# Optimization experiments

Hardware: AMD Instinct MI355X
Metric: run time of the kernel (lower is better)

Reference implementation:

```python
import jax, jax.numpy as jnp
import numpy as np


def _glorot(key, shape):
    fan_in, fan_out = shape[0], shape[1]
    lim = float(np.sqrt(6.0 / (fan_in + fan_out)))
    return jax.random.uniform(key, shape, jnp.float32, -lim, lim)


def setup_inputs() -> dict:
    key = jax.random.key(0)
    ks = jax.random.split(key, 17)
    B, P, F = 32, 9045, 750  # batch, pairs-per-subject, feature dim
    x = jax.random.normal(ks[0], (B, P, F), jnp.float32)
    # SimilarityMeasureNetwork: 750 -> 32 -> 16 -> 8 -> 1
    sw1 = _glorot(ks[1], (750, 32)); sb1 = jnp.zeros((32,), jnp.float32)
    sw2 = _glorot(ks[2], (32, 16));  sb2 = jnp.zeros((16,), jnp.float32)
    sw3 = _glorot(ks[3], (16, 8));   sb3 = jnp.zeros((8,), jnp.float32)
    sw4 = _glorot(ks[4], (8, 1));    sb4 = jnp.zeros((1,), jnp.float32)
    # ClassificationNet: 9045 -> 1024 -> 256 -> 64 -> 3
    cw1 = _glorot(ks[5], (9045, 1024)); cb1 = jnp.zeros((1024,), jnp.float32)
    cw2 = _glorot(ks[6], (1024, 256));  cb2 = jnp.zeros((256,), jnp.float32)
    cw3 = _glorot(ks[7], (256, 64));    cb3 = jnp.zeros((64,), jnp.float32)
    cw4 = _glorot(ks[8], (64, 3));      cb4 = jnp.zeros((3,), jnp.float32)
    return dict(x=x, sw1=sw1, sb1=sb1, sw2=sw2, sb2=sb2, sw3=sw3, sb3=sb3,
                sw4=sw4, sb4=sb4, cw1=cw1, cb1=cb1, cw2=cw2, cb2=cb2,
                cw3=cw3, cb3=cb3, cw4=cw4, cb4=cb4)


def reference(x, sw1, sb1, sw2, sb2, sw3, sb3, sw4, sb4,
              cw1, cb1, cw2, cb2, cw3, cb3, cw4, cb4):
    # Similarity MLP, batched over all (subject, pair) rows at once.
    # Dropout layers are identity at inference.
    h = jax.nn.relu(jnp.einsum('bpf,fk->bpk', x, sw1) + sb1)   # [B,P,32]
    h = jax.nn.relu(h @ sw2 + sb2)                              # [B,P,16]
    h = jax.nn.relu(h @ sw3 + sb3)                              # [B,P,8]
    sim = jnp.tanh(h @ sw4 + sb4)[..., 0]                        # [B,P]
    # Classification MLP on the per-subject similarity vector.
    c = jax.nn.relu(sim @ cw1 + cb1)                             # [B,1024]
    c = jax.nn.relu(c @ cw2 + cb2)                               # [B,256]
    c = jax.nn.relu(c @ cw3 + cb3)                               # [B,64]
    logits = c @ cw4 + cb4                                       # [B,3]
    return jax.nn.log_softmax(logits, axis=1)
```

## Files before the change

kernel.cpp:

```cpp
#include <hip/hip_runtime.h>
#include <stdint.h>
#include <stddef.h>

#define BB 32
#define PP 9045
#define FF 750
#define MM (BB*PP)
#define NT16 (MM/16)

typedef float  f32x4  __attribute__((ext_vector_type(4)));
typedef short  s16x8  __attribute__((ext_vector_type(8)));
typedef unsigned int u32x4v __attribute__((ext_vector_type(4)));

__device__ __forceinline__ unsigned rne_bf16(float f){
    unsigned u = __builtin_bit_cast(unsigned, f);
    return (u + 0x7fffu + ((u >> 16) & 1u)) >> 16;
}
__device__ __forceinline__ unsigned pack2(float lo, float hi){
    return rne_bf16(lo) | (rne_bf16(hi) << 16);
}
__device__ __forceinline__ float tanh_fast(float v){
    return 1.f - 2.f / (1.f + __expf(2.f * v));
}

__global__ void k_w1f(const float* __restrict__ sw1, u32x4v* __restrict__ w1f){
    int t = blockIdx.x * blockDim.x + threadIdx.x;
    if (t >= 24*2*64) return;
    int lane = t & 63, nt = (t >> 6) & 1, s = t >> 7;
    int col = nt*16 + (lane & 15);
    int kb  = s*32 + ((lane >> 4) << 3);
    float v[8];
    #pragma unroll
    for (int e = 0; e < 8; ++e){ int k = kb + e; v[e] = (k < FF) ? sw1[k*32 + col] : 0.f; }
    u32x4v o;
    o.x = pack2(v[0],v[1]); o.y = pack2(v[2],v[3]);
    o.z = pack2(v[4],v[5]); o.w = pack2(v[6],v[7]);
    w1f[t] = o;
}

__global__ __launch_bounds__(256) void k_sim(
    const float* __restrict__ x, const u32x4v* __restrict__ w1f,
    const float* __restrict__ sb1,
    const float* __restrict__ sw2, const float* __restrict__ sb2,
    const float* __restrict__ sw3, const float* __restrict__ sb3,
    const float* __restrict__ sw4, const float* __restrict__ sb4,
    float* __restrict__ simT)
{
    __shared__ __align__(16) unsigned short h1buf[4][16*40];
    __shared__ __align__(16) unsigned short h2buf[4][16*40];
    const int wid  = threadIdx.x >> 6;
    const int lane = threadIdx.x & 63;
    for (int i = lane; i < 16*40; i += 64) h2buf[wid][i] = 0;
    const int tile = blockIdx.x*4 + wid;
    if (tile >= NT16) return;
    const int g = lane >> 4;
    const int c = lane & 15;
    const int r0 = tile << 4;
    const int row = r0 + c;

    u32x4v t2, t3;
    {
        float v[8];
        #pragma unroll
        for (int e = 0; e < 8; ++e) v[e] = sw2[(8*g+e)*16 + c];
        t2.x = pack2(v[0],v[1]); t2.y = pack2(v[2],v[3]);
        t2.z = pack2(v[4],v[5]); t2.w = pack2(v[6],v[7]);
        #pragma unroll
        for (int e = 0; e < 8; ++e){
            int k = 8*g+e;
            v[e] = (k < 16 && c < 8) ? sw3[k*8 + c] : 0.f;
        }
        t3.x = pack2(v[0],v[1]); t3.y = pack2(v[2],v[3]);
        t3.z = pack2(v[4],v[5]); t3.w = pack2(v[6],v[7]);
    }
    const s16x8 w2f = __builtin_bit_cast(s16x8, t2);
    const s16x8 w3f = __builtin_bit_cast(s16x8, t3);
    const float w4c  = (c < 8) ? sw4[c] : 0.f;
    const float sb4v = sb4[0];
    const float b2c  = sb2[c];
    const float b3c  = (c < 8) ? sb3[c] : 0.f;

    f32x4 acc0, acc1;
    { float b0 = sb1[c], b1 = sb1[16+c];
      acc0 = (f32x4){b0,b0,b0,b0}; acc1 = (f32x4){b1,b1,b1,b1}; }

    const float2* xr = reinterpret_cast<const float2*>(x + (size_t)row*FF) + g*4;
    const u32x4v* wf = w1f + lane;

    #pragma unroll 4
    for (int s = 0; s < 23; ++s){
        float2 p0 = xr[16*s+0], p1 = xr[16*s+1], p2 = xr[16*s+2], p3 = xr[16*s+3];
        u32x4v a;
        a.x = pack2(p0.x,p0.y); a.y = pack2(p1.x,p1.y);
        a.z = pack2(p2.x,p2.y); a.w = pack2(p3.x,p3.y);
        s16x8 av  = __builtin_bit_cast(s16x8, a);
        s16x8 bv0 = __builtin_bit_cast(s16x8, wf[(2*s+0)*64]);
        s16x8 bv1 = __builtin_bit_cast(s16x8, wf[(2*s+1)*64]);
        acc0 = __builtin_amdgcn_mfma_f32_16x16x32_bf16(av, bv0, acc0, 0,0,0);
        acc1 = __builtin_amdgcn_mfma_f32_16x16x32_bf16(av, bv1, acc1, 0,0,0);
    }
    {
        int kb = 736 + g*8;
        float v[8];
        #pragma unroll
        for (int e = 0; e < 8; ++e){
            int k = kb + e;
            v[e] = (k < FF) ? x[(size_t)row*FF + k] : 0.f;
        }
        u32x4v a;
        a.x = pack2(v[0],v[1]); a.y = pack2(v[2],v[3]);
        a.z = pack2(v[4],v[5]); a.w = pack2(v[6],v[7]);
        s16x8 av  = __builtin_bit_cast(s16x8, a);
        s16x8 bv0 = __builtin_bit_cast(s16x8, wf[46*64]);
        s16x8 bv1 = __builtin_bit_cast(s16x8, wf[47*64]);
        acc0 = __builtin_amdgcn_mfma_f32_16x16x32_bf16(av, bv0, acc0, 0,0,0);
        acc1 = __builtin_amdgcn_mfma_f32_16x16x32_bf16(av, bv1, acc1, 0,0,0);
    }

    unsigned short* h1 = h1buf[wid];
    #pragma unroll
    for (int j = 0; j < 4; ++j){
        h1[(4*g+j)*40 + c]      = (unsigned short)rne_bf16(fmaxf(acc0[j], 0.f));
        h1[(4*g+j)*40 + 16 + c] = (unsigned short)rne_bf16(fmaxf(acc1[j], 0.f));
    }
    asm volatile("s_waitcnt lgkmcnt(0)" ::: "memory");
    s16x8 a2 = *reinterpret_cast<const s16x8*>(&h1[c*40 + 8*g]);
    f32x4 c2i = {b2c,b2c,b2c,b2c};
    f32x4 d2 = __builtin_amdgcn_mfma_f32_16x16x32_bf16(a2, w2f, c2i, 0,0,0);

    unsigned short* h2 = h2buf[wid];
    #pragma unroll
    for (int j = 0; j < 4; ++j)
        h2[(4*g+j)*40 + c] = (unsigned short)rne_bf16(fmaxf(d2[j], 0.f));
    asm volatile("s_waitcnt lgkmcnt(0)" ::: "memory");
    s16x8 a3 = *reinterpret_cast<const s16x8*>(&h2[c*40 + 8*g]);
    f32x4 c3i = {b3c,b3c,b3c,b3c};
    f32x4 d3 = __builtin_amdgcn_mfma_f32_16x16x32_bf16(a3, w3f, c3i, 0,0,0);

    #pragma unroll
    for (int j = 0; j < 4; ++j){
        float t = fmaxf(d3[j], 0.f) * w4c;
        t += __shfl_xor(t, 1);
        t += __shfl_xor(t, 2);
        t += __shfl_xor(t, 4);
        t += __shfl_xor(t, 8);
        if (c == 0){
            int grow = r0 + 4*g + j;
            int b = grow / PP;
            int p = grow - b*PP;
            simT[p*32 + b] = tanh_fast(t + sb4v);
        }
    }
}

__global__ __launch_bounds__(256) void k_c1(
    const float* __restrict__ simT, const float* __restrict__ cw1,
    float* __restrict__ c1)
{
    const int nb = blockIdx.x & 7;
    const int ks = blockIdx.x >> 3;
    const int t  = threadIdx.x;
    const int n  = nb*128 + (t & 127);
    const int kh = t >> 7;
    const int k0 = ks*283;
    const int k1 = (k0 + 283 < PP) ? k0 + 283 : PP;
    float acc[BB];
    #pragma unroll
    for (int b = 0; b < BB; ++b) acc[b] = 0.f;
    for (int k = k0 + kh; k < k1; k += 2){
        float w = cw1[(size_t)k*1024 + n];
        const float* sp = simT + k*32;
        #pragma unroll
        for (int b = 0; b < BB; ++b) acc[b] = fmaf(sp[b], w, acc[b]);
    }
    #pragma unroll
    for (int b = 0; b < BB; ++b) atomicAdd(c1 + b*1024 + n, acc[b]);
}

__global__ __launch_bounds__(256) void k_cls(
    const float* __restrict__ c1raw, const float* __restrict__ cb1,
    const float* __restrict__ cw2,  const float* __restrict__ cb2,
    const float* __restrict__ cw3,  const float* __restrict__ cb3,
    const float* __restrict__ cw4,  const float* __restrict__ cb4,
    float* __restrict__ out)
{
    __shared__ __align__(16) float c1s[1024];
    __shared__ float c2s[256];
    __shared__ float c3s[64];
    __shared__ float lgs[3];
    const int b = blockIdx.x, t = threadIdx.x;
    #pragma unroll
    for (int i = 0; i < 4; ++i){
        int n = i*256 + t;
        c1s[n] = fmaxf(c1raw[b*1024 + n] + cb1[n], 0.f);
    }
    __syncthreads();
    {
        float a = cb2[t];
        for (int k = 0; k < 1024; k += 4){
            float4 cv = *reinterpret_cast<const float4*>(&c1s[k]);
            a = fmaf(cv.x, cw2[(k+0)*256 + t], a);
            a = fmaf(cv.y, cw2[(k+1)*256 + t], a);
            a = fmaf(cv.z, cw2[(k+2)*256 + t], a);
            a = fmaf(cv.w, cw2[(k+3)*256 + t], a);
        }
        c2s[t] = fmaxf(a, 0.f);
    }
    __syncthreads();
    if (t < 64){
        float a = cb3[t];
        for (int k = 0; k < 256; ++k) a = fmaf(c2s[k], cw3[k*64 + t], a);
        c3s[t] = fmaxf(a, 0.f);
    }
    __syncthreads();
    if (t < 3){
        float a = cb4[t];
        for (int k = 0; k < 64; ++k) a = fmaf(c3s[k], cw4[k*3 + t], a);
        lgs[t] = a;
    }
    __syncthreads();
    if (t < 3){
        float m = fmaxf(fmaxf(lgs[0], lgs[1]), lgs[2]);
        float s = __expf(lgs[0]-m) + __expf(lgs[1]-m) + __expf(lgs[2]-m);
        out[b*3 + t] = lgs[t] - m - __logf(s);
    }
}

extern "C" void kernel_launch(void* const* d_in, const int* in_sizes, int n_in,
                              void* d_out, int out_size, void* d_ws, size_t ws_size,
                              hipStream_t stream) {
    const float* x   = (const float*)d_in[0];
    const float* sw1 = (const float*)d_in[1];
    const float* sb1 = (const float*)d_in[2];
    const float* sw2 = (const float*)d_in[3];
    const float* sb2 = (const float*)d_in[4];
    const float* sw3 = (const float*)d_in[5];
    const float* sb3 = (const float*)d_in[6];
    const float* sw4 = (const float*)d_in[7];
    const float* sb4 = (const float*)d_in[8];
    const float* cw1 = (const float*)d_in[9];
    const float* cb1 = (const float*)d_in[10];
    const float* cw2 = (const float*)d_in[11];
    const float* cb2 = (const float*)d_in[12];
    const float* cw3 = (const float*)d_in[13];
    const float* cb3 = (const float*)d_in[14];
    const float* cw4 = (const float*)d_in[15];
    const float* cb4 = (const float*)d_in[16];

    char* ws = (char*)d_ws;
    u32x4v* w1f = (u32x4v*)ws;
    float* simT = (float*)(ws + (64<<10));
    float* c1   = (float*)(ws + (64<<10) + 1310720);

    hipMemsetAsync(c1, 0, BB*1024*sizeof(float), stream);
    k_w1f<<<12, 256, 0, stream>>>(sw1, w1f);
    k_sim<<<(NT16 + 3)/4, 256, 0, stream>>>(x, w1f, sb1, sw2, sb2, sw3, sb3,
                                            sw4, sb4, simT);
    k_c1 <<<256, 256, 0, stream>>>(simT, cw1, c1);
    k_cls<<<BB, 256, 0, stream>>>(c1, cb1, cw2, cb2, cw3, cb3, cw4, cb4,
                                  (float*)d_out);
}
```

Measured before the change: 338.0 us.

## Stream x through LDS with async global_load_lds triple buffering; drop atomics

The main similarity GEMM loop now stages x tiles into per-wave LDS with global_load_lds in a three-deep pipeline. Swizzled addressing is meant to avoid bank conflicts, and the W1 fragments are prefetched by inline asm loads with manual vmcnt waits. Conversion to bf16 uses the hardware v_cvt_pk_bf16_f32 instruction instead of software rounding. The classifier first layer writes per-split partial sums that k_cls reduces, replacing the atomics and the memset. The risks are the fragile hand-tuned waitcnt ordering and extra partial-buffer traffic in k_cls.

```diff
diff --git a/kernel.cpp b/kernel.cpp
--- a/kernel.cpp
+++ b/kernel.cpp
@@ -12,12 +12,21 @@
 typedef short  s16x8  __attribute__((ext_vector_type(8)));
 typedef unsigned int u32x4v __attribute__((ext_vector_type(4)));
 
+typedef const __attribute__((address_space(1))) void* gp1;
+typedef __attribute__((address_space(3))) void* sp3;
+typedef __attribute__((address_space(3))) unsigned char* sp3c;
+
 __device__ __forceinline__ unsigned rne_bf16(float f){
     unsigned u = __builtin_bit_cast(unsigned, f);
     return (u + 0x7fffu + ((u >> 16) & 1u)) >> 16;
 }
 __device__ __forceinline__ unsigned pack2(float lo, float hi){
     return rne_bf16(lo) | (rne_bf16(hi) << 16);
+}
+__device__ __forceinline__ unsigned cvtpk(float lo, float hi){
+    unsigned r;
+    asm volatile("v_cvt_pk_bf16_f32 %0, %1, %2" : "=v"(r) : "v"(lo), "v"(hi));
+    return r;
 }
 __device__ __forceinline__ float tanh_fast(float v){
     return 1.f - 2.f / (1.f + __expf(2.f * v));
@@ -46,17 +55,15 @@
     const float* __restrict__ sw4, const float* __restrict__ sb4,
     float* __restrict__ simT)
 {
-    __shared__ __align__(16) unsigned short h1buf[4][16*40];
-    __shared__ __align__(16) unsigned short h2buf[4][16*40];
+    __shared__ __attribute__((aligned(16))) unsigned char scratch[4*6144];
     const int wid  = threadIdx.x >> 6;
     const int lane = threadIdx.x & 63;
-    for (int i = lane; i < 16*40; i += 64) h2buf[wid][i] = 0;
     const int tile = blockIdx.x*4 + wid;
     if (tile >= NT16) return;
     const int g = lane >> 4;
     const int c = lane & 15;
     const int r0 = tile << 4;
-    const int row = r0 + c;
+    const unsigned wbase = (unsigned)wid * 6144u;
 
     u32x4v t2, t3;
     {
@@ -84,40 +91,101 @@
     { float b0 = sb1[c], b1 = sb1[16+c];
       acc0 = (f32x4){b0,b0,b0,b0}; acc1 = (f32x4){b1,b1,b1,b1}; }
 
-    const float2* xr = reinterpret_cast<const float2*>(x + (size_t)row*FF) + g*4;
-    const u32x4v* wf = w1f + lane;
-
-    #pragma unroll 4
-    for (int s = 0; s < 23; ++s){
-        float2 p0 = xr[16*s+0], p1 = xr[16*s+1], p2 = xr[16*s+2], p3 = xr[16*s+3];
-        u32x4v a;
-        a.x = pack2(p0.x,p0.y); a.y = pack2(p1.x,p1.y);
-        a.z = pack2(p2.x,p2.y); a.w = pack2(p3.x,p3.y);
-        s16x8 av  = __builtin_bit_cast(s16x8, a);
-        s16x8 bv0 = __builtin_bit_cast(s16x8, wf[(2*s+0)*64]);
-        s16x8 bv1 = __builtin_bit_cast(s16x8, wf[(2*s+1)*64]);
-        acc0 = __builtin_amdgcn_mfma_f32_16x16x32_bf16(av, bv0, acc0, 0,0,0);
-        acc1 = __builtin_amdgcn_mfma_f32_16x16x32_bf16(av, bv1, acc1, 0,0,0);
-    }
-    {
+    const int rr = lane >> 3;
+    const unsigned so = (unsigned)(((lane & 7) << 4) ^ ((rr & 3) << 4));
+    const char* src0 = (const char*)x + (size_t)(r0 + rr) * 3000u + so;
+    const char* src1 = src0 + 24000;
+
+    unsigned char* ldsg = scratch;
+    const uint32_t lbase = (uint32_t)(uintptr_t)(sp3c)scratch;
+    const uint32_t sw = ((uint32_t)(c & 3)) << 4;
+    const uint32_t rb0 = lbase + wbase + (uint32_t)c*128u + ((32u*(uint32_t)g) ^ sw);
+    const uint32_t rb1 = lbase + wbase + (uint32_t)c*128u + (((32u*(uint32_t)g) + 16u) ^ sw);
+
+    const unsigned long long wbw = (unsigned long long)(uintptr_t)w1f + (unsigned)lane*16u;
+
+    u32x4v WA[3], WB[3];
+
+#define GLLP(BUFOFS, STEP) do{ \
+    __builtin_amdgcn_global_load_lds((gp1)(src0 + 128*(STEP)), (sp3)(ldsg + wbase + (BUFOFS)), 16, 0, 0); \
+    __builtin_amdgcn_global_load_lds((gp1)(src1 + 128*(STEP)), (sp3)(ldsg + wbase + (BUFOFS) + 1024), 16, 0, 0); \
+}while(0)
+
+#define W1FLD(SLOT, STEP) do{ \
+    unsigned long long wa_ = wbw + (unsigned)(2048*(STEP)); \
+    asm volatile("global_load_dwordx4 %0, %1, off" : "=&v"(WA[SLOT]) : "v"(wa_)); \
+    asm volatile("global_load_dwordx4 %0, %1, off offset:1024" : "=&v"(WB[SLOT]) : "v"(wa_)); \
+}while(0)
+
+#define PACK_MFMA(D0, D1, SLOT) do{ \
+    u32x4v a_; \
+    a_.x = cvtpk((D0)[0], (D0)[1]); a_.y = cvtpk((D0)[2], (D0)[3]); \
+    a_.z = cvtpk((D1)[0], (D1)[1]); a_.w = cvtpk((D1)[2], (D1)[3]); \
+    s16x8 av_ = __builtin_bit_cast(s16x8, a_); \
+    acc0 = __builtin_amdgcn_mfma_f32_16x16x32_bf16(av_, __builtin_bit_cast(s16x8, WA[SLOT]), acc0, 0,0,0); \
+    acc1 = __builtin_amdgcn_mfma_f32_16x16x32_bf16(av_, __builtin_bit_cast(s16x8, WB[SLOT]), acc1, 0,0,0); \
+}while(0)
+
+    GLLP(0,    0);
+    W1FLD(0,   0);
+    GLLP(2048, 1);
+    W1FLD(1,   1);
+    GLLP(4096, 2);
+
+#pragma unroll
+    for (int s = 0; s < 21; ++s){
+        asm volatile("s_waitcnt vmcnt(6)");
+        f32x4 d0, d1;
+        const uint32_t off = (uint32_t)((s % 3) * 2048);
+        asm volatile("ds_read_b128 %0, %1" : "=v"(d0) : "v"(rb0 + off));
+        asm volatile("ds_read_b128 %0, %1" : "=v"(d1) : "v"(rb1 + off));
+        W1FLD((s + 2) % 3, s + 2);
+        asm volatile("s_waitcnt lgkmcnt(0)");
+        __builtin_amdgcn_sched_barrier(0);
+        if (s < 20) GLLP((s % 3) * 2048, s + 3);
+        PACK_MFMA(d0, d1, s % 3);
+    }
+    {
+        asm volatile("s_waitcnt vmcnt(4)");
+        f32x4 d0, d1;
+        asm volatile("ds_read_b128 %0, %1" : "=v"(d0) : "v"(rb0));
+        asm volatile("ds_read_b128 %0, %1" : "=v"(d1) : "v"(rb1));
+        W1FLD(2, 23);
+        asm volatile("s_waitcnt lgkmcnt(0)");
+        __builtin_amdgcn_sched_barrier(0);
+        PACK_MFMA(d0, d1, 0);
+    }
+    {
+        asm volatile("s_waitcnt vmcnt(2)");
+        f32x4 d0, d1;
+        asm volatile("ds_read_b128 %0, %1" : "=v"(d0) : "v"(rb0 + 2048u));
+        asm volatile("ds_read_b128 %0, %1" : "=v"(d1) : "v"(rb1 + 2048u));
+        asm volatile("s_waitcnt lgkmcnt(0)" ::: "memory");
+        __builtin_amdgcn_sched_barrier(0);
+        PACK_MFMA(d0, d1, 1);
+    }
+    {
+        asm volatile("s_waitcnt vmcnt(0)" ::: "memory");
+        __builtin_amdgcn_sched_barrier(0);
         int kb = 736 + g*8;
         float v[8];
         #pragma unroll
         for (int e = 0; e < 8; ++e){
             int k = kb + e;
-            v[e] = (k < FF) ? x[(size_t)row*FF + k] : 0.f;
+            v[e] = (k < FF) ? x[(size_t)(r0 + c)*FF + k] : 0.f;
         }
         u32x4v a;
         a.x = pack2(v[0],v[1]); a.y = pack2(v[2],v[3]);
         a.z = pack2(v[4],v[5]); a.w = pack2(v[6],v[7]);
-        s16x8 av  = __builtin_bit_cast(s16x8, a);
-        s16x8 bv0 = __builtin_bit_cast(s16x8, wf[46*64]);
-        s16x8 bv1 = __builtin_bit_cast(s16x8, wf[47*64]);
-        acc0 = __builtin_amdgcn_mfma_f32_16x16x32_bf16(av, bv0, acc0, 0,0,0);
-        acc1 = __builtin_amdgcn_mfma_f32_16x16x32_bf16(av, bv1, acc1, 0,0,0);
-    }
-
-    unsigned short* h1 = h1buf[wid];
+        s16x8 av = __builtin_bit_cast(s16x8, a);
+        acc0 = __builtin_amdgcn_mfma_f32_16x16x32_bf16(av, __builtin_bit_cast(s16x8, WA[2]), acc0, 0,0,0);
+        acc1 = __builtin_amdgcn_mfma_f32_16x16x32_bf16(av, __builtin_bit_cast(s16x8, WB[2]), acc1, 0,0,0);
+    }
+
+    unsigned short* h1 = (unsigned short*)(scratch + wbase);
+    unsigned short* h2 = (unsigned short*)(scratch + wbase + 2048);
+    for (int i = lane; i < 640; i += 64) h2[i] = 0;
+
     #pragma unroll
     for (int j = 0; j < 4; ++j){
         h1[(4*g+j)*40 + c]      = (unsigned short)rne_bf16(fmaxf(acc0[j], 0.f));
@@ -128,7 +196,6 @@
     f32x4 c2i = {b2c,b2c,b2c,b2c};
     f32x4 d2 = __builtin_amdgcn_mfma_f32_16x16x32_bf16(a2, w2f, c2i, 0,0,0);
 
-    unsigned short* h2 = h2buf[wid];
     #pragma unroll
     for (int j = 0; j < 4; ++j)
         h2[(4*g+j)*40 + c] = (unsigned short)rne_bf16(fmaxf(d2[j], 0.f));
@@ -151,11 +218,14 @@
             simT[p*32 + b] = tanh_fast(t + sb4v);
         }
     }
+#undef GLLP
+#undef W1FLD
+#undef PACK_MFMA
 }
 
 __global__ __launch_bounds__(256) void k_c1(
     const float* __restrict__ simT, const float* __restrict__ cw1,
-    float* __restrict__ c1)
+    float* __restrict__ part)
 {
     const int nb = blockIdx.x & 7;
     const int ks = blockIdx.x >> 3;
@@ -173,18 +243,19 @@
         #pragma unroll
         for (int b = 0; b < BB; ++b) acc[b] = fmaf(sp[b], w, acc[b]);
     }
-    #pragma unroll
-    for (int b = 0; b < BB; ++b) atomicAdd(c1 + b*1024 + n, acc[b]);
+    float* dst = part + (size_t)((ks << 1) | kh) * (BB * 1024) + n;
+    #pragma unroll
+    for (int b = 0; b < BB; ++b) dst[b*1024] = acc[b];
 }
 
 __global__ __launch_bounds__(256) void k_cls(
-    const float* __restrict__ c1raw, const float* __restrict__ cb1,
+    const float* __restrict__ part, const float* __restrict__ cb1,
     const float* __restrict__ cw2,  const float* __restrict__ cb2,
     const float* __restrict__ cw3,  const float* __restrict__ cb3,
     const float* __restrict__ cw4,  const float* __restrict__ cb4,
     float* __restrict__ out)
 {
-    __shared__ __align__(16) float c1s[1024];
+    __shared__ __attribute__((aligned(16))) float c1s[1024];
     __shared__ float c2s[256];
     __shared__ float c3s[64];
     __shared__ float lgs[3];
@@ -192,7 +263,10 @@
     #pragma unroll
     for (int i = 0; i < 4; ++i){
         int n = i*256 + t;
-        c1s[n] = fmaxf(c1raw[b*1024 + n] + cb1[n], 0.f);
+        float a = 0.f;
+        #pragma unroll 8
+        for (int q = 0; q < 64; ++q) a += part[(size_t)q*(BB*1024) + b*1024 + n];
+        c1s[n] = fmaxf(a + cb1[n], 0.f);
     }
     __syncthreads();
     {
@@ -246,17 +320,17 @@
     const float* cb3 = (const float*)d_in[14];
     const float* cw4 = (const float*)d_in[15];
     const float* cb4 = (const float*)d_in[16];
+    (void)in_sizes; (void)n_in; (void)out_size; (void)ws_size;
 
     char* ws = (char*)d_ws;
-    u32x4v* w1f = (u32x4v*)ws;
-    float* simT = (float*)(ws + (64<<10));
-    float* c1   = (float*)(ws + (64<<10) + 1310720);
-
-    hipMemsetAsync(c1, 0, BB*1024*sizeof(float), stream);
+    u32x4v* w1f  = (u32x4v*)ws;
+    float*  simT = (float*)(ws + (64<<10));
+    float*  part = (float*)(ws + (2<<20));
+
     k_w1f<<<12, 256, 0, stream>>>(sw1, w1f);
     k_sim<<<(NT16 + 3)/4, 256, 0, stream>>>(x, w1f, sb1, sw2, sb2, sw3, sb3,
                                             sw4, sb4, simT);
-    k_c1 <<<256, 256, 0, stream>>>(simT, cw1, c1);
-    k_cls<<<BB, 256, 0, stream>>>(c1, cb1, cw2, cb2, cw3, cb3, cw4, cb4,
+    k_c1 <<<256, 256, 0, stream>>>(simT, cw1, part);
+    k_cls<<<BB, 256, 0, stream>>>(part, cb1, cw2, cb2, cw3, cb3, cw4, cb4,
                                   (float*)d_out);
 }
```

New measurement: 358.4 us. +6.0%, slower.

## Stage x through LDS with async global_load_lds double buffering and replace atomics with partials

Applied to the files above, without the earlier changes.

The similarity kernel now streams x tiles into a swizzled per-wave LDS scratch with global_load_lds and double buffering. It prefetches the bf16 W1 fragments into registers across windows and uses the v_cvt_pk_bf16_f32 instruction for packing. The aim is to overlap the large x stream with MFMA work and get coalesced loads. Separately, the c1 split-K atomics and memset are replaced by per-slice partial buffers that the classifier kernel sums, which removes atomic traffic but adds 64 partial reads per output. The large per-block LDS footprint (64KB) together with launch_bounds(256,2) limits occupancy.

```diff
diff --git a/kernel.cpp b/kernel.cpp
--- a/kernel.cpp
+++ b/kernel.cpp
@@ -12,12 +12,21 @@
 typedef short  s16x8  __attribute__((ext_vector_type(8)));
 typedef unsigned int u32x4v __attribute__((ext_vector_type(4)));
 
+typedef const __attribute__((address_space(1))) void* gp1;
+typedef __attribute__((address_space(3))) void* sp3;
+typedef __attribute__((address_space(3))) unsigned char* sp3c;
+
 __device__ __forceinline__ unsigned rne_bf16(float f){
     unsigned u = __builtin_bit_cast(unsigned, f);
     return (u + 0x7fffu + ((u >> 16) & 1u)) >> 16;
 }
 __device__ __forceinline__ unsigned pack2(float lo, float hi){
     return rne_bf16(lo) | (rne_bf16(hi) << 16);
+}
+__device__ __forceinline__ unsigned cvtpk(float lo, float hi){
+    unsigned r;
+    asm volatile("v_cvt_pk_bf16_f32 %0, %1, %2" : "=v"(r) : "v"(lo), "v"(hi));
+    return r;
 }
 __device__ __forceinline__ float tanh_fast(float v){
     return 1.f - 2.f / (1.f + __expf(2.f * v));
@@ -38,7 +47,7 @@
     w1f[t] = o;
 }
 
-__global__ __launch_bounds__(256) void k_sim(
+__global__ __launch_bounds__(256, 2) void k_sim(
     const float* __restrict__ x, const u32x4v* __restrict__ w1f,
     const float* __restrict__ sb1,
     const float* __restrict__ sw2, const float* __restrict__ sb2,
@@ -46,17 +55,15 @@
     const float* __restrict__ sw4, const float* __restrict__ sb4,
     float* __restrict__ simT)
 {
-    __shared__ __align__(16) unsigned short h1buf[4][16*40];
-    __shared__ __align__(16) unsigned short h2buf[4][16*40];
+    __shared__ __attribute__((aligned(16))) unsigned char scratch[4*16384];
     const int wid  = threadIdx.x >> 6;
     const int lane = threadIdx.x & 63;
-    for (int i = lane; i < 16*40; i += 64) h2buf[wid][i] = 0;
     const int tile = blockIdx.x*4 + wid;
     if (tile >= NT16) return;
     const int g = lane >> 4;
     const int c = lane & 15;
     const int r0 = tile << 4;
-    const int row = r0 + c;
+    const unsigned wbase = (unsigned)wid * 16384u;
 
     u32x4v t2, t3;
     {
@@ -84,40 +91,84 @@
     { float b0 = sb1[c], b1 = sb1[16+c];
       acc0 = (f32x4){b0,b0,b0,b0}; acc1 = (f32x4){b1,b1,b1,b1}; }
 
-    const float2* xr = reinterpret_cast<const float2*>(x + (size_t)row*FF) + g*4;
-    const u32x4v* wf = w1f + lane;
-
-    #pragma unroll 4
-    for (int s = 0; s < 23; ++s){
-        float2 p0 = xr[16*s+0], p1 = xr[16*s+1], p2 = xr[16*s+2], p3 = xr[16*s+3];
-        u32x4v a;
-        a.x = pack2(p0.x,p0.y); a.y = pack2(p1.x,p1.y);
-        a.z = pack2(p2.x,p2.y); a.w = pack2(p3.x,p3.y);
-        s16x8 av  = __builtin_bit_cast(s16x8, a);
-        s16x8 bv0 = __builtin_bit_cast(s16x8, wf[(2*s+0)*64]);
-        s16x8 bv1 = __builtin_bit_cast(s16x8, wf[(2*s+1)*64]);
-        acc0 = __builtin_amdgcn_mfma_f32_16x16x32_bf16(av, bv0, acc0, 0,0,0);
-        acc1 = __builtin_amdgcn_mfma_f32_16x16x32_bf16(av, bv1, acc1, 0,0,0);
-    }
-    {
-        int kb = 736 + g*8;
-        float v[8];
-        #pragma unroll
-        for (int e = 0; e < 8; ++e){
-            int k = kb + e;
-            v[e] = (k < FF) ? x[(size_t)row*FF + k] : 0.f;
-        }
-        u32x4v a;
-        a.x = pack2(v[0],v[1]); a.y = pack2(v[2],v[3]);
-        a.z = pack2(v[4],v[5]); a.w = pack2(v[6],v[7]);
-        s16x8 av  = __builtin_bit_cast(s16x8, a);
-        s16x8 bv0 = __builtin_bit_cast(s16x8, wf[46*64]);
-        s16x8 bv1 = __builtin_bit_cast(s16x8, wf[47*64]);
-        acc0 = __builtin_amdgcn_mfma_f32_16x16x32_bf16(av, bv0, acc0, 0,0,0);
-        acc1 = __builtin_amdgcn_mfma_f32_16x16x32_bf16(av, bv1, acc1, 0,0,0);
-    }
-
-    unsigned short* h1 = h1buf[wid];
+    const int h  = lane >> 5;
+    const unsigned t16 = (unsigned)(lane & 31) << 4;
+    const char* xb = (const char*)x + (size_t)(r0 + h) * 3000u;
+
+    const uint32_t lbase = (uint32_t)(uintptr_t)(sp3c)scratch + wbase;
+    const uint32_t S = ((uint32_t)(c & 7)) << 4;
+
+    const unsigned long long wfb = (unsigned long long)(uintptr_t)w1f + (unsigned)lane*16u;
+
+    u32x4v WFA[3][4], WFB[3][4];
+    f32x4 D0[4], D1[4];
+
+#define STAGE(QOFF, BUFSEL) do{ \
+    _Pragma("unroll") \
+    for (int j_ = 0; j_ < 8; ++j_){ \
+        unsigned swz_ = t16 ^ ((unsigned)((2*j_ + h) & 7) << 4); \
+        __builtin_amdgcn_global_load_lds((gp1)(xb + (QOFF) + 6000*j_ + swz_), \
+            (sp3)(scratch + wbase + (unsigned)((BUFSEL)*8192) + (unsigned)(1024*j_)), 16, 0, 0); \
+    } \
+}while(0)
+
+#define WFLD(Q, B) do{ \
+    unsigned long long a_ = wfb + (unsigned)(8192*(Q)); \
+    asm volatile("global_load_dwordx4 %0, %1, off"             : "=&v"(WFA[B][0]) : "v"(a_)); \
+    asm volatile("global_load_dwordx4 %0, %1, off offset:1024" : "=&v"(WFB[B][0]) : "v"(a_)); \
+    asm volatile("global_load_dwordx4 %0, %1, off offset:2048" : "=&v"(WFA[B][1]) : "v"(a_)); \
+    asm volatile("global_load_dwordx4 %0, %1, off offset:3072" : "=&v"(WFB[B][1]) : "v"(a_)); \
+    unsigned long long a2_ = a_ + 4096u; \
+    asm volatile("global_load_dwordx4 %0, %1, off"             : "=&v"(WFA[B][2]) : "v"(a2_)); \
+    asm volatile("global_load_dwordx4 %0, %1, off offset:1024" : "=&v"(WFB[B][2]) : "v"(a2_)); \
+    asm volatile("global_load_dwordx4 %0, %1, off offset:2048" : "=&v"(WFA[B][3]) : "v"(a2_)); \
+    asm volatile("global_load_dwordx4 %0, %1, off offset:3072" : "=&v"(WFB[B][3]) : "v"(a2_)); \
+}while(0)
+
+#define WINDOW(Q, BANK, VMSTR, ...) do{ \
+    asm volatile("s_waitcnt vmcnt(" VMSTR ")"); \
+    { \
+      const uint32_t bb_ = lbase + (uint32_t)(((Q)&1)*8192) + (uint32_t)c*512u; \
+      _Pragma("unroll") \
+      for (int ks_ = 0; ks_ < 4; ++ks_){ \
+          uint32_t u0_ = ((uint32_t)(128*ks_) + 32u*(uint32_t)g) ^ S; \
+          uint32_t u1_ = ((uint32_t)(128*ks_) + 32u*(uint32_t)g + 16u) ^ S; \
+          asm volatile("ds_read_b128 %0, %1" : "=&v"(D0[ks_]) : "v"(bb_ + u0_)); \
+          asm volatile("ds_read_b128 %0, %1" : "=&v"(D1[ks_]) : "v"(bb_ + u1_)); \
+      } \
+    } \
+    asm volatile("s_waitcnt lgkmcnt(0)"); \
+    __builtin_amdgcn_sched_barrier(0); \
+    __VA_ARGS__ \
+    _Pragma("unroll") \
+    for (int ks_ = 0; ks_ < 4; ++ks_){ \
+        u32x4v a_; \
+        a_.x = cvtpk(D0[ks_][0], D0[ks_][1]); a_.y = cvtpk(D0[ks_][2], D0[ks_][3]); \
+        a_.z = cvtpk(D1[ks_][0], D1[ks_][1]); a_.w = cvtpk(D1[ks_][2], D1[ks_][3]); \
+        s16x8 av_ = __builtin_bit_cast(s16x8, a_); \
+        acc0 = __builtin_amdgcn_mfma_f32_16x16x32_bf16(av_, __builtin_bit_cast(s16x8, WFA[BANK][ks_]), acc0, 0,0,0); \
+        acc1 = __builtin_amdgcn_mfma_f32_16x16x32_bf16(av_, __builtin_bit_cast(s16x8, WFB[BANK][ks_]), acc1, 0,0,0); \
+    } \
+}while(0)
+
+    STAGE(0,    0); WFLD(0, 0);
+    STAGE(512,  1); WFLD(1, 1);
+
+    WINDOW(0, 0, "16", STAGE(1024, 0); WFLD(2, 2); );
+    WINDOW(1, 1, "16", STAGE(1536, 1); WFLD(3, 0); );
+    WINDOW(2, 2, "16", STAGE(2048, 0); WFLD(4, 1); );
+    WINDOW(3, 0, "16", STAGE(2560, 1); WFLD(5, 2); );
+    WINDOW(4, 1, "16", ; );
+    WINDOW(5, 2, "0",
+        if (g >= 2){ D0[3] = (f32x4){0.f,0.f,0.f,0.f}; D1[3] = (f32x4){0.f,0.f,0.f,0.f}; }
+        else if (g == 1){ D1[3][2] = 0.f; D1[3][3] = 0.f; } );
+
+    asm volatile("" ::: "memory");
+
+    unsigned short* h1 = (unsigned short*)(scratch + wbase);
+    unsigned short* h2 = (unsigned short*)(scratch + wbase + 2048);
+    for (int i = lane; i < 640; i += 64) h2[i] = 0;
+
     #pragma unroll
     for (int j = 0; j < 4; ++j){
         h1[(4*g+j)*40 + c]      = (unsigned short)rne_bf16(fmaxf(acc0[j], 0.f));
@@ -128,7 +179,6 @@
     f32x4 c2i = {b2c,b2c,b2c,b2c};
     f32x4 d2 = __builtin_amdgcn_mfma_f32_16x16x32_bf16(a2, w2f, c2i, 0,0,0);
 
-    unsigned short* h2 = h2buf[wid];
     #pragma unroll
     for (int j = 0; j < 4; ++j)
         h2[(4*g+j)*40 + c] = (unsigned short)rne_bf16(fmaxf(d2[j], 0.f));
@@ -151,11 +201,14 @@
             simT[p*32 + b] = tanh_fast(t + sb4v);
         }
     }
+#undef STAGE
+#undef WFLD
+#undef WINDOW
 }
 
 __global__ __launch_bounds__(256) void k_c1(
     const float* __restrict__ simT, const float* __restrict__ cw1,
-    float* __restrict__ c1)
+    float* __restrict__ part)
 {
     const int nb = blockIdx.x & 7;
     const int ks = blockIdx.x >> 3;
@@ -173,18 +226,19 @@
         #pragma unroll
         for (int b = 0; b < BB; ++b) acc[b] = fmaf(sp[b], w, acc[b]);
     }
-    #pragma unroll
-    for (int b = 0; b < BB; ++b) atomicAdd(c1 + b*1024 + n, acc[b]);
+    float* dst = part + (size_t)((ks << 1) | kh) * (BB * 1024) + n;
+    #pragma unroll
+    for (int b = 0; b < BB; ++b) dst[b*1024] = acc[b];
 }
 
 __global__ __launch_bounds__(256) void k_cls(
-    const float* __restrict__ c1raw, const float* __restrict__ cb1,
+    const float* __restrict__ part, const float* __restrict__ cb1,
     const float* __restrict__ cw2,  const float* __restrict__ cb2,
     const float* __restrict__ cw3,  const float* __restrict__ cb3,
     const float* __restrict__ cw4,  const float* __restrict__ cb4,
     float* __restrict__ out)
 {
-    __shared__ __align__(16) float c1s[1024];
+    __shared__ __attribute__((aligned(16))) float c1s[1024];
     __shared__ float c2s[256];
     __shared__ float c3s[64];
     __shared__ float lgs[3];
@@ -192,7 +246,10 @@
     #pragma unroll
     for (int i = 0; i < 4; ++i){
         int n = i*256 + t;
-        c1s[n] = fmaxf(c1raw[b*1024 + n] + cb1[n], 0.f);
+        float a = 0.f;
+        #pragma unroll 8
+        for (int q = 0; q < 64; ++q) a += part[(size_t)q*(BB*1024) + b*1024 + n];
+        c1s[n] = fmaxf(a + cb1[n], 0.f);
     }
     __syncthreads();
     {
@@ -246,17 +303,17 @@
     const float* cb3 = (const float*)d_in[14];
     const float* cw4 = (const float*)d_in[15];
     const float* cb4 = (const float*)d_in[16];
+    (void)in_sizes; (void)n_in; (void)out_size; (void)ws_size;
 
     char* ws = (char*)d_ws;
-    u32x4v* w1f = (u32x4v*)ws;
-    float* simT = (float*)(ws + (64<<10));
-    float* c1   = (float*)(ws + (64<<10) + 1310720);
-
-    hipMemsetAsync(c1, 0, BB*1024*sizeof(float), stream);
+    u32x4v* w1f  = (u32x4v*)ws;
+    float*  simT = (float*)(ws + (64<<10));
+    float*  part = (float*)(ws + (2<<20));
+
     k_w1f<<<12, 256, 0, stream>>>(sw1, w1f);
     k_sim<<<(NT16 + 3)/4, 256, 0, stream>>>(x, w1f, sb1, sw2, sb2, sw3, sb3,
                                             sw4, sb4, simT);
-    k_c1 <<<256, 256, 0, stream>>>(simT, cw1, c1);
-    k_cls<<<BB, 256, 0, stream>>>(c1, cb1, cw2, cb2, cw3, cb3, cw4, cb4,
+    k_c1 <<<256, 256, 0, stream>>>(simT, cw1, part);
+    k_cls<<<BB, 256, 0, stream>>>(part, cb1, cw2, cb2, cw3, cb3, cw4, cb4,
                                   (float*)d_out);
 }
```

Result: faster. 331.2 us (-2.0%).
